# Performance work log

Hardware: AMD Instinct MI355X
Metric: run time of the kernel (lower is better)

The kernel has to match this reference:

```python
import jax, jax.numpy as jnp
import numpy as np
import math

K_BRANCH = 8  # config['k']

def _selectors(n, k):
    # Static (trace-time) construction of per-level gather indices, mask=True branch.
    L = math.ceil(math.log(n) / math.log(k)) + 1
    rel = [0] + [math.ceil(n / k ** i) for i in range(L)]  # level sizes, leaves first
    Li = np.cumsum(np.array(rel))                          # level start offsets in node dim
    sels = []
    for l in range(L):
        m = rel[l + 1]
        i = np.arange(m)[:, None]
        anc = None
        if l < L - 1:
            m_next = rel[l + 2]
            j = np.arange(m_next)[None, :]
            cond = (j + 1) / m_next <= i / m
            anc = np.where(cond, Li[l + 1] + j, 0)
        s = np.arange(k)[None, :]
        ridx = np.minimum(i // k * k + s, m - 1)
        sib = np.where(ridx <= i, Li[l] + ridx, 0)  # rel/m <= i/m  <=>  rel <= i
        chi = None
        if l >= 1:
            m_prev = rel[l]
            c = np.arange(k)[None, :]
            ridx = np.minimum(i * k + c, m_prev - 1)
            cond = ridx / m_prev <= i / m
            chi = np.where(cond, Li[l - 1] + ridx, 0)
        sels.append((anc, sib, chi))
    return L, Li, sels

def _sdp(q, Kmat, Vmat, sel, d):
    keys = Kmat[:, :, sel, :]   # [b,h,m,w,d] gather
    vals = Vmat[:, :, sel, :]
    logits = jnp.einsum('bhnd,bhnkd->bhnk', q, keys) / math.sqrt(d)
    w = jax.nn.softmax(logits, axis=-1)
    return jnp.einsum('bhnk,bhnkd->bhnd', w, vals)

def setup_inputs() -> dict:
    key = jax.random.key(0)
    k1, k2, k3 = jax.random.split(key, 3)
    b, h, n_tot, d = 2, 4, 585, 128
    return {
        'Q': jax.random.normal(k1, (b, h, n_tot, d), dtype=jnp.float32),
        'K': jax.random.normal(k2, (b, h, n_tot, d), dtype=jnp.float32),
        'V': jax.random.normal(k3, (b, h, n_tot, d), dtype=jnp.float32),
        'n': 512,
    }

def reference(Q, K, V, n):
    k = K_BRANCH
    d = Q.shape[-1]
    L, Li, sels = _selectors(int(n), k)
    # Sequential bottom-up level updates: V at level l is rewritten before level l+1 reads it.
    for l in range(L):
        anc, sib, chi = sels[l]
        q = Q[:, :, Li[l]:Li[l + 1], :]
        out = _sdp(q, K, V, sib, d)
        if anc is not None:
            out = out + _sdp(q, K, V, anc, d)
        if chi is not None:
            out = out + _sdp(q, K, V, chi, d)
        V = V.at[:, :, Li[l]:Li[l + 1], :].set(out / 3.0)
    return V
```

## Files before the change

kernel.cpp:

```cpp
#include <hip/hip_runtime.h>
#include <math.h>

#define D 128
#define NTOT 585
#define SCALE 0.08838834764831845f
#define THIRD 0.33333333333333333f

__device__ __forceinline__ float rsum_c(float v) {
    v += __shfl_xor(v, 1, 64);
    v += __shfl_xor(v, 2, 64);
    v += __shfl_xor(v, 4, 64);
    return v;
}
__device__ __forceinline__ float rsum_s(float v) {
    v += __shfl_xor(v, 8, 64);
    v += __shfl_xor(v, 16, 64);
    v += __shfl_xor(v, 32, 64);
    return v;
}
__device__ __forceinline__ float rmax_s(float v) {
    v = fmaxf(v, __shfl_xor(v, 8, 64));
    v = fmaxf(v, __shfl_xor(v, 16, 64));
    v = fmaxf(v, __shfl_xor(v, 32, 64));
    return v;
}
__device__ __forceinline__ float dot16(const float4 q[4], const float* __restrict__ row, int c) {
    const float4* k = (const float4*)(row + (c << 4));
    float4 k0 = k[0], k1 = k[1], k2 = k[2], k3 = k[3];
    float p0 = q[0].x * k0.x + q[0].y * k0.y + q[0].z * k0.z + q[0].w * k0.w;
    float p1 = q[1].x * k1.x + q[1].y * k1.y + q[1].z * k1.z + q[1].w * k1.w;
    float p2 = q[2].x * k2.x + q[2].y * k2.y + q[2].z * k2.z + q[2].w * k2.w;
    float p3 = q[3].x * k3.x + q[3].y * k3.y + q[3].z * k3.z + q[3].w * k3.w;
    return (p0 + p1) + (p2 + p3);
}
__device__ __forceinline__ void vacc(float w, const float* __restrict__ row, int c, float4 acc[4]) {
    const float4* v = (const float4*)(row + (c << 4));
#pragma unroll
    for (int u = 0; u < 4; ++u) {
        float4 t = v[u];
        acc[u].x += w * t.x; acc[u].y += w * t.y; acc[u].z += w * t.z; acc[u].w += w * t.w;
    }
}
__device__ __forceinline__ void attend(const float4 q[4], const float* __restrict__ krow,
                                       const float* __restrict__ vrow, int c, float4 acc[4]) {
    float lg = rsum_c(dot16(q, krow, c)) * SCALE;
    float m = rmax_s(lg);
    float e = __expf(lg - m);
    float z = rsum_s(e);
    vacc(e / z, vrow, c, acc);
}
__device__ __forceinline__ void attend_reg(const float4 q[4], const float* __restrict__ krow,
                                           const float4 vv[4], int c, float4 acc[4]) {
    float lg = rsum_c(dot16(q, krow, c)) * SCALE;
    float m = rmax_s(lg);
    float e = __expf(lg - m);
    float z = rsum_s(e);
    const float w = e / z;
#pragma unroll
    for (int u = 0; u < 4; ++u) {
        acc[u].x += w * vv[u].x; acc[u].y += w * vv[u].y;
        acc[u].z += w * vv[u].z; acc[u].w += w * vv[u].w;
    }
}
__device__ __forceinline__ void loadq(const float* __restrict__ qrow, int c, float4 q[4]) {
    const float4* qp = (const float4*)(qrow + (c << 4));
#pragma unroll
    for (int u = 0; u < 4; ++u) q[u] = qp[u];
}
__device__ __forceinline__ void butterfly_acc(float4 acc[4]) {
#pragma unroll
    for (int u = 0; u < 4; ++u) {
        acc[u].x = rsum_s(acc[u].x);
        acc[u].y = rsum_s(acc[u].y);
        acc[u].z = rsum_s(acc[u].z);
        acc[u].w = rsum_s(acc[u].w);
    }
}

__device__ __forceinline__ void l0_compute(int i, int s, int c,
                                           const float* __restrict__ Qb,
                                           const float* __restrict__ Kb,
                                           const float* __restrict__ Vb,
                                           float4 acc[4]) {
    float4 q4[4];
    loadq(Qb + (size_t)i * D, c, q4);
#pragma unroll
    for (int u = 0; u < 4; ++u) acc[u] = make_float4(0.f, 0.f, 0.f, 0.f);
    {
        const int r = (i & ~7) + s;
        const int idx = (r <= i) ? r : 0;
        attend(q4, Kb + (size_t)idx * D, Vb + (size_t)idx * D, c, acc);
    }
    {
        float lg[8];
        int idx[8];
#pragma unroll
        for (int r = 0; r < 8; ++r) {
            const int j = 8 * r + s;
            idx[r] = (8 * (j + 1) <= i) ? (512 + j) : 0;
            lg[r] = rsum_c(dot16(q4, Kb + (size_t)idx[r] * D, c)) * SCALE;
        }
        float m = lg[0];
#pragma unroll
        for (int r = 1; r < 8; ++r) m = fmaxf(m, lg[r]);
        m = rmax_s(m);
        float z = 0.f;
#pragma unroll
        for (int r = 0; r < 8; ++r) { lg[r] = __expf(lg[r] - m); z += lg[r]; }
        z = rsum_s(z);
        const float inv = 1.f / z;
#pragma unroll
        for (int r = 0; r < 8; ++r) vacc(lg[r] * inv, Vb + (size_t)idx[r] * D, c, acc);
    }
    butterfly_acc(acc);
}

__global__ __launch_bounds__(256) void sequoia_onepass(const float* __restrict__ Q,
                                                       const float* __restrict__ K,
                                                       const float* __restrict__ V,
                                                       float* __restrict__ Out) {
    const int gwave = (blockIdx.x * 256 + threadIdx.x) >> 6;
    const int lane = threadIdx.x & 63;
    const int s = lane >> 3, c = lane & 7;

    if (gwave < 4096) {
        const int i = gwave & 511;
        const int bh = gwave >> 9;
        const float* Qb = Q + (size_t)bh * NTOT * D;
        const float* Kb = K + (size_t)bh * NTOT * D;
        const float* Vb = V + (size_t)bh * NTOT * D;
        float* Ob = Out + (size_t)bh * NTOT * D;
        float4 acc[4];
        l0_compute(i, s, c, Qb, Kb, Vb, acc);
        if (s == 0) {
            float4* orow = (float4*)(Ob + (size_t)i * D + (c << 4));
#pragma unroll
            for (int u = 0; u < 4; ++u)
                orow[u] = make_float4(acc[u].x * THIRD, acc[u].y * THIRD,
                                      acc[u].z * THIRD, acc[u].w * THIRD);
        }
        return;
    }

    const int t = gwave - 4096;
    const int i = t & 63;
    const int bh = t >> 6;
    const float* Qb = Q + (size_t)bh * NTOT * D;
    const float* Kb = K + (size_t)bh * NTOT * D;
    const float* Vb = V + (size_t)bh * NTOT * D;
    float* Ob = Out + (size_t)bh * NTOT * D;

    float4 v0n[4];
    {
        const float4* vp = (const float4*)(Vb + (c << 4));
#pragma unroll
        for (int u = 0; u < 4; ++u) {
            float4 v = vp[u];
            v0n[u] = make_float4(v.x * (2.f * THIRD), v.y * (2.f * THIRD),
                                 v.z * (2.f * THIRD), v.w * (2.f * THIRD));
        }
    }

    float4 o0[4];
    if (i == 0) {
#pragma unroll
        for (int u = 0; u < 4; ++u) o0[u] = v0n[u];
    } else {
        float4 tmp[4];
        l0_compute(8 * i, s, c, Qb, Kb, Vb, tmp);
#pragma unroll
        for (int u = 0; u < 4; ++u)
            o0[u] = make_float4(tmp[u].x * THIRD, tmp[u].y * THIRD,
                                tmp[u].z * THIRD, tmp[u].w * THIRD);
    }

    float4 o1[4];
    {
        float4 q4[4];
        loadq(Qb + (size_t)(512 + i) * D, c, q4);
        float4 acc[4] = {{0,0,0,0},{0,0,0,0},{0,0,0,0},{0,0,0,0}};
        {
            const int r = (i & ~7) + s;
            const bool pass = (r <= i);
            const float* krow = Kb + (size_t)(pass ? 512 + r : 0) * D;
            float4 vv[4];
            if (pass) {
                const float4* vp = (const float4*)(Vb + (size_t)(512 + r) * D + (c << 4));
#pragma unroll
                for (int u = 0; u < 4; ++u) vv[u] = vp[u];
            } else {
#pragma unroll
                for (int u = 0; u < 4; ++u) vv[u] = v0n[u];
            }
            attend_reg(q4, krow, vv, c, acc);
        }
        {
            const bool pass = (8 * (s + 1) <= i);
            const float* krow = Kb + (size_t)(pass ? 576 + s : 0) * D;
            float4 vv[4];
            if (pass) {
                const float4* vp = (const float4*)(Vb + (size_t)(576 + s) * D + (c << 4));
#pragma unroll
                for (int u = 0; u < 4; ++u) vv[u] = vp[u];
            } else {
#pragma unroll
                for (int u = 0; u < 4; ++u) vv[u] = v0n[u];
            }
            attend_reg(q4, krow, vv, c, acc);
        }
        {
            const float* krow = (s == 0) ? (Kb + (size_t)(8 * i) * D) : Kb;
            float4 vv[4];
#pragma unroll
            for (int u = 0; u < 4; ++u) vv[u] = (s == 0) ? o0[u] : v0n[u];
            attend_reg(q4, krow, vv, c, acc);
        }
        butterfly_acc(acc);
#pragma unroll
        for (int u = 0; u < 4; ++u)
            o1[u] = make_float4(acc[u].x * THIRD, acc[u].y * THIRD,
                                acc[u].z * THIRD, acc[u].w * THIRD);
        if (s == 0) {
            float4* orow = (float4*)(Ob + (size_t)(512 + i) * D + (c << 4));
#pragma unroll
            for (int u = 0; u < 4; ++u) orow[u] = o1[u];
        }
    }

    if ((i & 7) == 0) {
        const int j = i >> 3;
        float4 q2[4];
        loadq(Qb + (size_t)(576 + j) * D, c, q2);
        float4 acc[4] = {{0,0,0,0},{0,0,0,0},{0,0,0,0},{0,0,0,0}};
        {
            const bool pass = (s <= j);
            const float* krow = Kb + (size_t)(pass ? 576 + s : 0) * D;
            float4 vv[4];
            if (pass) {
                const float4* vp = (const float4*)(Vb + (size_t)(576 + s) * D + (c << 4));
#pragma unroll
                for (int u = 0; u < 4; ++u) vv[u] = vp[u];
            } else {
#pragma unroll
                for (int u = 0; u < 4; ++u) vv[u] = v0n[u];
            }
            attend_reg(q2, krow, vv, c, acc);
        }
        {
            const float* krow = (s == 0) ? (Kb + (size_t)(512 + 8 * j) * D) : Kb;
            float4 vv[4];
#pragma unroll
            for (int u = 0; u < 4; ++u) vv[u] = (s == 0) ? o1[u] : v0n[u];
            attend_reg(q2, krow, vv, c, acc);
        }
        butterfly_acc(acc);
        float4 o2[4];
#pragma unroll
        for (int u = 0; u < 4; ++u)
            o2[u] = make_float4((acc[u].x + v0n[u].x) * THIRD, (acc[u].y + v0n[u].y) * THIRD,
                                (acc[u].z + v0n[u].z) * THIRD, (acc[u].w + v0n[u].w) * THIRD);
        if (s == 0) {
            float4* orow = (float4*)(Ob + (size_t)(576 + j) * D + (c << 4));
#pragma unroll
            for (int u = 0; u < 4; ++u) orow[u] = o2[u];
        }

        if (j == 0) {
            float4 q3[4];
            loadq(Qb + (size_t)584 * D, c, q3);
            const float* krow = (s == 0) ? (Kb + (size_t)576 * D) : Kb;
            float lg = rsum_c(dot16(q3, krow, c)) * SCALE;
            float m = rmax_s(lg);
            float e = __expf(lg - m);
            float z = rsum_s(e);
            const float w = e / z;
            float4 acc3[4];
#pragma unroll
            for (int u = 0; u < 4; ++u) {
                float4 vv = (s == 0) ? o2[u] : v0n[u];
                acc3[u] = make_float4(w * vv.x, w * vv.y, w * vv.z, w * vv.w);
            }
            butterfly_acc(acc3);
            if (s == 0) {
                const float4* v584 = (const float4*)(Vb + (size_t)584 * D + (c << 4));
                float4* orow = (float4*)(Ob + (size_t)584 * D + (c << 4));
#pragma unroll
                for (int u = 0; u < 4; ++u) {
                    float4 bb = v584[u];
                    orow[u] = make_float4((acc3[u].x + bb.x) * THIRD,
                                          (acc3[u].y + bb.y) * THIRD,
                                          (acc3[u].z + bb.z) * THIRD,
                                          (acc3[u].w + bb.w) * THIRD);
                }
            }
        }
    }
}

extern "C" void kernel_launch(void* const* d_in, const int* in_sizes, int n_in,
                              void* d_out, int out_size, void* d_ws, size_t ws_size,
                              hipStream_t stream) {
    const float* Q = (const float*)d_in[0];
    const float* K = (const float*)d_in[1];
    const float* V = (const float*)d_in[2];
    float* Out = (float*)d_out;
    hipLaunchKernelGGL(sequoia_onepass, dim3(1152), dim3(256), 0, stream, Q, K, V, Out);
}
```

Baseline: 87.80 us.

## Collapse masked index-0 attention slots into one weighted term and skip their loads

Masked selector slots all gather node 0, so the kernel now computes the node-0 logit once and folds all masked slots into a single term with multiplicity weight, instead of loading and dotting K/V rows for each masked slot. The ancestor loop in level 0 skips whole row groups beyond the valid range, cutting redundant global loads and FMAs. Wave assignment is reordered so the upper-level waves come first. This adds more branches and divergence within a wave, and uses a -1e30 sentinel for masked lanes.

```diff
diff --git a/kernel.cpp b/kernel.cpp
--- a/kernel.cpp
+++ b/kernel.cpp
@@ -41,21 +41,7 @@
         acc[u].x += w * t.x; acc[u].y += w * t.y; acc[u].z += w * t.z; acc[u].w += w * t.w;
     }
 }
-__device__ __forceinline__ void attend(const float4 q[4], const float* __restrict__ krow,
-                                       const float* __restrict__ vrow, int c, float4 acc[4]) {
-    float lg = rsum_c(dot16(q, krow, c)) * SCALE;
-    float m = rmax_s(lg);
-    float e = __expf(lg - m);
-    float z = rsum_s(e);
-    vacc(e / z, vrow, c, acc);
-}
-__device__ __forceinline__ void attend_reg(const float4 q[4], const float* __restrict__ krow,
-                                           const float4 vv[4], int c, float4 acc[4]) {
-    float lg = rsum_c(dot16(q, krow, c)) * SCALE;
-    float m = rmax_s(lg);
-    float e = __expf(lg - m);
-    float z = rsum_s(e);
-    const float w = e / z;
+__device__ __forceinline__ void vacc_reg(float w, const float4 vv[4], float4 acc[4]) {
 #pragma unroll
     for (int u = 0; u < 4; ++u) {
         acc[u].x += w * vv[u].x; acc[u].y += w * vv[u].y;
@@ -77,40 +63,79 @@
     }
 }
 
-__device__ __forceinline__ void l0_compute(int i, int s, int c,
-                                           const float* __restrict__ Qb,
-                                           const float* __restrict__ Kb,
-                                           const float* __restrict__ Vb,
-                                           float4 acc[4]) {
+__device__ __forceinline__ void l0_slim(int i, int s, int c,
+                                        const float* __restrict__ Qb,
+                                        const float* __restrict__ Kb,
+                                        const float* __restrict__ Vb,
+                                        float4 acc[4]) {
     float4 q4[4];
     loadq(Qb + (size_t)i * D, c, q4);
 #pragma unroll
     for (int u = 0; u < 4; ++u) acc[u] = make_float4(0.f, 0.f, 0.f, 0.f);
+    const float lg0 = rsum_c(dot16(q4, Kb, c)) * SCALE;
+    const int sl = i & 7;
+    const int g = i >> 3;
+
     {
-        const int r = (i & ~7) + s;
-        const int idx = (r <= i) ? r : 0;
-        attend(q4, Kb + (size_t)idx * D, Vb + (size_t)idx * D, c, acc);
-    }
+        float lg = -1e30f;
+        if (s <= sl)
+            lg = rsum_c(dot16(q4, Kb + (size_t)(8 * g + s) * D, c)) * SCALE;
+        const float m = fmaxf(rmax_s(lg), lg0);
+        const float e = (s <= sl) ? __expf(lg - m) : 0.f;
+        const float e0 = __expf(lg0 - m);
+        float zp = e;
+        if (s == 0) zp += (float)(7 - sl) * e0;
+        const float inv = 1.f / rsum_s(zp);
+        if (s <= sl) vacc(e * inv, Vb + (size_t)(8 * g + s) * D, c, acc);
+        if (s == 0 && sl < 7) vacc((float)(7 - sl) * e0 * inv, Vb, c, acc);
+    }
+
     {
-        float lg[8];
-        int idx[8];
-#pragma unroll
-        for (int r = 0; r < 8; ++r) {
-            const int j = 8 * r + s;
-            idx[r] = (8 * (j + 1) <= i) ? (512 + j) : 0;
-            lg[r] = rsum_c(dot16(q4, Kb + (size_t)idx[r] * D, c)) * SCALE;
-        }
-        float m = lg[0];
-#pragma unroll
-        for (int r = 1; r < 8; ++r) m = fmaxf(m, lg[r]);
-        m = rmax_s(m);
-        float z = 0.f;
-#pragma unroll
-        for (int r = 0; r < 8; ++r) { lg[r] = __expf(lg[r] - m); z += lg[r]; }
-        z = rsum_s(z);
-        const float inv = 1.f / z;
-#pragma unroll
-        for (int r = 0; r < 8; ++r) vacc(lg[r] * inv, Vb + (size_t)idx[r] * D, c, acc);
+        float lgA[8];
+        float mloc = lg0;
+#pragma unroll
+        for (int R = 0; R < 4; ++R) {
+            if (16 * R < g) {
+#pragma unroll
+                for (int rr = 0; rr < 2; ++rr) {
+                    const int r = 2 * R + rr;
+                    const int j = 8 * r + s;
+                    float lg = -1e30f;
+                    if (j < g)
+                        lg = rsum_c(dot16(q4, Kb + (size_t)(512 + j) * D, c)) * SCALE;
+                    lgA[r] = lg;
+                    mloc = fmaxf(mloc, lg);
+                }
+            } else { lgA[2 * R] = -1e30f; lgA[2 * R + 1] = -1e30f; }
+        }
+        const float m = rmax_s(mloc);
+        const float e0 = __expf(lg0 - m);
+        float zp = (s == 0) ? (float)(64 - g) * e0 : 0.f;
+        float eA[8];
+#pragma unroll
+        for (int R = 0; R < 4; ++R) {
+            if (16 * R < g) {
+#pragma unroll
+                for (int rr = 0; rr < 2; ++rr) {
+                    const int r = 2 * R + rr;
+                    eA[r] = (lgA[r] > -1e29f) ? __expf(lgA[r] - m) : 0.f;
+                    zp += eA[r];
+                }
+            }
+        }
+        const float inv = 1.f / rsum_s(zp);
+#pragma unroll
+        for (int R = 0; R < 4; ++R) {
+            if (16 * R < g) {
+#pragma unroll
+                for (int rr = 0; rr < 2; ++rr) {
+                    const int r = 2 * R + rr;
+                    const int j = 8 * r + s;
+                    if (j < g) vacc(eA[r] * inv, Vb + (size_t)(512 + j) * D, c, acc);
+                }
+            }
+        }
+        if (s == 0) vacc((float)(64 - g) * e0 * inv, Vb, c, acc);
     }
     butterfly_acc(acc);
 }
@@ -123,15 +148,16 @@
     const int lane = threadIdx.x & 63;
     const int s = lane >> 3, c = lane & 7;
 
-    if (gwave < 4096) {
-        const int i = gwave & 511;
-        const int bh = gwave >> 9;
+    if (gwave >= 512) {
+        const int w = gwave - 512;
+        const int i = w & 511;
+        const int bh = w >> 9;
         const float* Qb = Q + (size_t)bh * NTOT * D;
         const float* Kb = K + (size_t)bh * NTOT * D;
         const float* Vb = V + (size_t)bh * NTOT * D;
         float* Ob = Out + (size_t)bh * NTOT * D;
         float4 acc[4];
-        l0_compute(i, s, c, Qb, Kb, Vb, acc);
+        l0_slim(i, s, c, Qb, Kb, Vb, acc);
         if (s == 0) {
             float4* orow = (float4*)(Ob + (size_t)i * D + (c << 4));
 #pragma unroll
@@ -142,7 +168,7 @@
         return;
     }
 
-    const int t = gwave - 4096;
+    const int t = gwave;
     const int i = t & 63;
     const int bh = t >> 6;
     const float* Qb = Q + (size_t)bh * NTOT * D;
@@ -167,7 +193,7 @@
         for (int u = 0; u < 4; ++u) o0[u] = v0n[u];
     } else {
         float4 tmp[4];
-        l0_compute(8 * i, s, c, Qb, Kb, Vb, tmp);
+        l0_slim(8 * i, s, c, Qb, Kb, Vb, tmp);
 #pragma unroll
         for (int u = 0; u < 4; ++u)
             o0[u] = make_float4(tmp[u].x * THIRD, tmp[u].y * THIRD,
@@ -176,44 +202,52 @@
 
     float4 o1[4];
     {
-        float4 q4[4];
-        loadq(Qb + (size_t)(512 + i) * D, c, q4);
+        float4 q1[4];
+        loadq(Qb + (size_t)(512 + i) * D, c, q1);
         float4 acc[4] = {{0,0,0,0},{0,0,0,0},{0,0,0,0},{0,0,0,0}};
+        const float lg0q = rsum_c(dot16(q1, Kb, c)) * SCALE;
+        const int sl1 = i & 7;
+        const int gq = i >> 3;
         {
             const int r = (i & ~7) + s;
-            const bool pass = (r <= i);
-            const float* krow = Kb + (size_t)(pass ? 512 + r : 0) * D;
-            float4 vv[4];
-            if (pass) {
-                const float4* vp = (const float4*)(Vb + (size_t)(512 + r) * D + (c << 4));
-#pragma unroll
-                for (int u = 0; u < 4; ++u) vv[u] = vp[u];
-            } else {
-#pragma unroll
-                for (int u = 0; u < 4; ++u) vv[u] = v0n[u];
-            }
-            attend_reg(q4, krow, vv, c, acc);
-        }
-        {
-            const bool pass = (8 * (s + 1) <= i);
-            const float* krow = Kb + (size_t)(pass ? 576 + s : 0) * D;
-            float4 vv[4];
-            if (pass) {
-                const float4* vp = (const float4*)(Vb + (size_t)(576 + s) * D + (c << 4));
-#pragma unroll
-                for (int u = 0; u < 4; ++u) vv[u] = vp[u];
-            } else {
-#pragma unroll
-                for (int u = 0; u < 4; ++u) vv[u] = v0n[u];
-            }
-            attend_reg(q4, krow, vv, c, acc);
-        }
-        {
-            const float* krow = (s == 0) ? (Kb + (size_t)(8 * i) * D) : Kb;
-            float4 vv[4];
-#pragma unroll
-            for (int u = 0; u < 4; ++u) vv[u] = (s == 0) ? o0[u] : v0n[u];
-            attend_reg(q4, krow, vv, c, acc);
+            float lg = -1e30f;
+            if (s <= sl1)
+                lg = rsum_c(dot16(q1, Kb + (size_t)(512 + r) * D, c)) * SCALE;
+            const float m = fmaxf(rmax_s(lg), lg0q);
+            const float e = (s <= sl1) ? __expf(lg - m) : 0.f;
+            const float e0 = __expf(lg0q - m);
+            float zp = e;
+            if (s == 0) zp += (float)(7 - sl1) * e0;
+            const float inv = 1.f / rsum_s(zp);
+            if (s <= sl1) vacc(e * inv, Vb + (size_t)(512 + r) * D, c, acc);
+            if (s == 0 && sl1 < 7) vacc_reg((float)(7 - sl1) * e0 * inv, v0n, acc);
+        }
+        {
+            float lg = -1e30f;
+            if (s < gq)
+                lg = rsum_c(dot16(q1, Kb + (size_t)(576 + s) * D, c)) * SCALE;
+            const float m = fmaxf(rmax_s(lg), lg0q);
+            const float e = (s < gq) ? __expf(lg - m) : 0.f;
+            const float e0 = __expf(lg0q - m);
+            float zp = e;
+            if (s == 0) zp += (float)(8 - gq) * e0;
+            const float inv = 1.f / rsum_s(zp);
+            if (s < gq) vacc(e * inv, Vb + (size_t)(576 + s) * D, c, acc);
+            if (s == 0) vacc_reg((float)(8 - gq) * e0 * inv, v0n, acc);
+        }
+        {
+            float lg = -1e30f;
+            if (s == 0)
+                lg = rsum_c(dot16(q1, Kb + (size_t)(8 * i) * D, c)) * SCALE;
+            const float m = fmaxf(rmax_s(lg), lg0q);
+            const float e = (s == 0) ? __expf(lg - m) : 0.f;
+            const float e0 = __expf(lg0q - m);
+            const float zp = (s == 0) ? (e + 7.f * e0) : 0.f;
+            const float inv = 1.f / rsum_s(zp);
+            if (s == 0) {
+                vacc_reg(e * inv, o0, acc);
+                vacc_reg(7.f * e0 * inv, v0n, acc);
+            }
         }
         butterfly_acc(acc);
 #pragma unroll
@@ -232,26 +266,33 @@
         float4 q2[4];
         loadq(Qb + (size_t)(576 + j) * D, c, q2);
         float4 acc[4] = {{0,0,0,0},{0,0,0,0},{0,0,0,0},{0,0,0,0}};
-        {
-            const bool pass = (s <= j);
-            const float* krow = Kb + (size_t)(pass ? 576 + s : 0) * D;
-            float4 vv[4];
-            if (pass) {
-                const float4* vp = (const float4*)(Vb + (size_t)(576 + s) * D + (c << 4));
-#pragma unroll
-                for (int u = 0; u < 4; ++u) vv[u] = vp[u];
-            } else {
-#pragma unroll
-                for (int u = 0; u < 4; ++u) vv[u] = v0n[u];
-            }
-            attend_reg(q2, krow, vv, c, acc);
-        }
-        {
-            const float* krow = (s == 0) ? (Kb + (size_t)(512 + 8 * j) * D) : Kb;
-            float4 vv[4];
-#pragma unroll
-            for (int u = 0; u < 4; ++u) vv[u] = (s == 0) ? o1[u] : v0n[u];
-            attend_reg(q2, krow, vv, c, acc);
+        const float lg0q = rsum_c(dot16(q2, Kb, c)) * SCALE;
+        {
+            float lg = -1e30f;
+            if (s <= j)
+                lg = rsum_c(dot16(q2, Kb + (size_t)(576 + s) * D, c)) * SCALE;
+            const float m = fmaxf(rmax_s(lg), lg0q);
+            const float e = (s <= j) ? __expf(lg - m) : 0.f;
+            const float e0 = __expf(lg0q - m);
+            float zp = e;
+            if (s == 0) zp += (float)(7 - j) * e0;
+            const float inv = 1.f / rsum_s(zp);
+            if (s <= j) vacc(e * inv, Vb + (size_t)(576 + s) * D, c, acc);
+            if (s == 0 && j < 7) vacc_reg((float)(7 - j) * e0 * inv, v0n, acc);
+        }
+        {
+            float lg = -1e30f;
+            if (s == 0)
+                lg = rsum_c(dot16(q2, Kb + (size_t)(512 + 8 * j) * D, c)) * SCALE;
+            const float m = fmaxf(rmax_s(lg), lg0q);
+            const float e = (s == 0) ? __expf(lg - m) : 0.f;
+            const float e0 = __expf(lg0q - m);
+            const float zp = (s == 0) ? (e + 7.f * e0) : 0.f;
+            const float inv = 1.f / rsum_s(zp);
+            if (s == 0) {
+                vacc_reg(e * inv, o1, acc);
+                vacc_reg(7.f * e0 * inv, v0n, acc);
+            }
         }
         butterfly_acc(acc);
         float4 o2[4];
@@ -268,17 +309,19 @@
         if (j == 0) {
             float4 q3[4];
             loadq(Qb + (size_t)584 * D, c, q3);
-            const float* krow = (s == 0) ? (Kb + (size_t)576 * D) : Kb;
-            float lg = rsum_c(dot16(q3, krow, c)) * SCALE;
-            float m = rmax_s(lg);
-            float e = __expf(lg - m);
-            float z = rsum_s(e);
-            const float w = e / z;
-            float4 acc3[4];
-#pragma unroll
-            for (int u = 0; u < 4; ++u) {
-                float4 vv = (s == 0) ? o2[u] : v0n[u];
-                acc3[u] = make_float4(w * vv.x, w * vv.y, w * vv.z, w * vv.w);
+            const float lg0q = rsum_c(dot16(q3, Kb, c)) * SCALE;
+            float lg = -1e30f;
+            if (s == 0)
+                lg = rsum_c(dot16(q3, Kb + (size_t)576 * D, c)) * SCALE;
+            const float m = fmaxf(rmax_s(lg), lg0q);
+            const float e = (s == 0) ? __expf(lg - m) : 0.f;
+            const float e0 = __expf(lg0q - m);
+            const float zp = (s == 0) ? (e + 7.f * e0) : 0.f;
+            const float inv = 1.f / rsum_s(zp);
+            float4 acc3[4] = {{0,0,0,0},{0,0,0,0},{0,0,0,0},{0,0,0,0}};
+            if (s == 0) {
+                vacc_reg(e * inv, o2, acc3);
+                vacc_reg(7.f * e0 * inv, v0n, acc3);
             }
             butterfly_acc(acc3);
             if (s == 0) {
```

Result: faster. 85.29 us (-2.9%).
